# Kernel optimization log

Measured on AMD Instinct MI355X. Metric: run time of the kernel, lower is better.

The kernel has to match this reference:

```python
import jax, jax.numpy as jnp
import numpy as np

B, D, K, H = 131072, 256, 8, 128

def setup_inputs() -> dict:
    key = jax.random.key(0)
    ks = jax.random.split(key, 8)
    z = jax.random.normal(ks[0], (B, D), dtype=jnp.float32)
    logits = jax.random.normal(ks[1], (B, K), dtype=jnp.float32)
    regime_probs = jax.nn.softmax(logits, axis=-1)  # rows sum to 1, per docstring
    s1 = 1.0 / np.sqrt(D)
    s2 = 1.0 / np.sqrt(H)
    W1 = jax.random.uniform(ks[2], (K, D, H), jnp.float32, -s1, s1)
    b1 = jax.random.uniform(ks[3], (K, H), jnp.float32, -s1, s1)
    W2 = jax.random.uniform(ks[4], (K, H, H), jnp.float32, -s2, s2)
    b2 = jax.random.uniform(ks[5], (K, H), jnp.float32, -s2, s2)
    W3 = jax.random.uniform(ks[6], (K, H), jnp.float32, -s2, s2)   # final Linear(H,1) weight
    b3 = jax.random.uniform(ks[7], (K,), jnp.float32, -s2, s2)
    return {"z": z, "regime_probs": regime_probs, "W1": W1, "b1": b1,
            "W2": W2, "b2": b2, "W3": W3, "b3": b3}

def reference(z, regime_probs, W1, b1, W2, b2, W3, b3):
    # All K experts evaluated densely as grouped GEMMs (torch ran them in a Python loop).
    # GELU is exact erf-based (torch nn.GELU default). Dropout=0 -> identity.
    h = jax.nn.gelu(jnp.einsum('bd,kdh->bkh', z, W1) + b1, approximate=False)   # (B,K,H)
    h = jax.nn.gelu(jnp.einsum('bkh,khg->bkg', h, W2) + b2, approximate=False)  # (B,K,H)
    expert_preds = jnp.einsum('bkh,kh->bk', h, W3) + b3                          # (B,K)
    blended = jnp.sum(regime_probs * expert_preds, axis=1)                       # (B,)
    return (blended, expert_preds)
```

## Files before the change

kernel.cpp:

```cpp
#include <hip/hip_runtime.h>
#include <hip/hip_bf16.h>
#include <stdint.h>

#define B_ROWS 131072
#define DD 256
#define KEXP 8
#define HH 128
#define BM 64
#define NW 4

typedef float  f32x4  __attribute__((ext_vector_type(4)));
typedef short  bf16x8 __attribute__((ext_vector_type(8)));

__device__ __forceinline__ unsigned short f2bf(float f) {
    __bf16 h = (__bf16)f;
    return __builtin_bit_cast(unsigned short, h);
}

__device__ __forceinline__ float gelu_erf(float x) {
    float s = x * 0.70710678118654752f;
    float a = fabsf(s);
    float t = __builtin_amdgcn_rcpf(fmaf(0.47047f, a, 1.0f));
    float p = fmaf(t, 0.7478556f, -0.0958798f);
    p = fmaf(t, p, 0.3480242f);
    float e = __expf(-a * a);
    float Q = p * t * e;
    float sel = (s >= 0.f) ? (2.0f - Q) : Q;
    return 0.5f * x * sel;
}

__device__ __forceinline__ bf16x8 gelu_pack(f32x4 lo, f32x4 hi) {
    bf16x8 r;
    r[0] = f2bf(gelu_erf(lo[0])); r[1] = f2bf(gelu_erf(lo[1]));
    r[2] = f2bf(gelu_erf(lo[2])); r[3] = f2bf(gelu_erf(lo[3]));
    r[4] = f2bf(gelu_erf(hi[0])); r[5] = f2bf(gelu_erf(hi[1]));
    r[6] = f2bf(gelu_erf(hi[2])); r[7] = f2bf(gelu_erf(hi[3]));
    return r;
}

__global__ void convert_weights(const float* __restrict__ W1, const float* __restrict__ W2,
                                uint16_t* __restrict__ w1o, uint16_t* __restrict__ w2o) {
    int idx = blockIdx.x * blockDim.x + threadIdx.x;
    const int total1 = KEXP * HH * DD;
    if (idx < total1) {
        int k    = idx >> 15;
        int rem  = idx & 32767;
        int q    = rem >> 13;
        int r2   = rem & 8191;
        int frag = r2 >> 9;
        int r3   = r2 & 511;
        int lane = r3 >> 3;
        int j    = r3 & 7;
        int kk   = frag >> 1;
        int hb   = frag & 1;
        int g    = lane >> 4;
        int c    = lane & 15;
        int d    = kk * 32 + g * 8 + j;
        int h    = q * 32 + hb * 16 + c;
        w1o[idx] = f2bf(W1[(k * DD + d) * HH + h]);
        return;
    }
    int idx2 = idx - total1;
    const int total2 = KEXP * HH * HH;
    if (idx2 < total2) {
        int k    = idx2 >> 14;
        int rem  = idx2 & 16383;
        int half = rem >> 13;
        int r2   = rem & 8191;
        int frag = r2 >> 9;
        int r3   = r2 & 511;
        int lane = r3 >> 3;
        int j    = r3 & 7;
        int kk2  = frag >> 2;
        int blk  = frag & 3;
        int g    = lane >> 4;
        int c    = lane & 15;
        int kl   = kk2 * 32 + g * 8 + j;
        int h    = (kl & ~0x1C) | ((kl & 4) << 2) | ((kl & 0x18) >> 1);
        int g2   = half * 64 + blk * 16 + c;
        w2o[idx2] = f2bf(W2[(k * HH + h) * HH + g2]);
    }
}

__device__ __forceinline__ void stage16k(const uint16_t* __restrict__ src, uint16_t* dst,
                                         int wave, int lane) {
    const char* s = (const char*)src + wave * 1024 + lane * 16;
    char* d = (char*)dst + wave * 1024;
    #pragma unroll
    for (int i = 0; i < 4; ++i)
        __builtin_amdgcn_global_load_lds(
            (const __attribute__((address_space(1))) void*)(s + i * 4096),
            (__attribute__((address_space(3))) void*)(d + i * 4096), 16, 0, 0);
}

__global__ __launch_bounds__(256, 4)
void moe_kernel(const float* __restrict__ z, const float* __restrict__ probs,
                const float* __restrict__ b1, const float* __restrict__ b2,
                const float* __restrict__ W3, const float* __restrict__ b3,
                const uint16_t* __restrict__ w1b, const uint16_t* __restrict__ w2b,
                float* __restrict__ out) {
    __shared__ __align__(16) uint16_t wbuf[2][8192];
    __shared__ __align__(16) float preds_lds[BM * KEXP];

    const int tid  = threadIdx.x;
    const int wave = tid >> 6;
    const int lane = tid & 63;
    const int c    = lane & 15;
    const int g    = lane >> 4;
    const int wg   = blockIdx.x;
    const long rowbase = (long)wg * BM;

    bf16x8 zf[8];
    {
        const float* zr = z + (rowbase + wave * 16 + c) * DD;
        #pragma unroll
        for (int kk = 0; kk < 8; ++kk) {
            const float* p = zr + kk * 32 + g * 8;
            float4 x0 = *(const float4*)(p);
            float4 x1 = *(const float4*)(p + 4);
            bf16x8 f;
            f[0] = f2bf(x0.x); f[1] = f2bf(x0.y); f[2] = f2bf(x0.z); f[3] = f2bf(x0.w);
            f[4] = f2bf(x1.x); f[5] = f2bf(x1.y); f[6] = f2bf(x1.z); f[7] = f2bf(x1.w);
            zf[kk] = f;
        }
    }

    stage16k(w1b, wbuf[0], wave, lane);
    __syncthreads();

    int cur = 0;

    for (int ke = 0; ke < KEXP; ++ke) {
        bf16x8 pa[4];
        const uint16_t* w1e = w1b + ke * (HH * DD);
        const uint16_t* w2e = w2b + ke * (HH * HH);
        const float* bb1 = b1 + ke * HH;

        #pragma unroll
        for (int q = 0; q < 4; ++q) {
            if (q < 3) stage16k(w1e + (q + 1) * 8192, wbuf[cur ^ 1], wave, lane);
            else       stage16k(w2e,                  wbuf[cur ^ 1], wave, lane);

            f32x4 a0 = *(const f32x4*)(bb1 + 32 * q +  0 + 4 * g);
            f32x4 a1 = *(const f32x4*)(bb1 + 32 * q + 16 + 4 * g);
            const bf16x8* fb = (const bf16x8*)(wbuf[cur]) + lane;
            #pragma unroll
            for (int kk = 0; kk < 8; ++kk) {
                a0 = __builtin_amdgcn_mfma_f32_16x16x32_bf16(fb[kk * 128     ], zf[kk], a0, 0, 0, 0);
                a1 = __builtin_amdgcn_mfma_f32_16x16x32_bf16(fb[kk * 128 + 64], zf[kk], a1, 0, 0, 0);
            }
            pa[q] = gelu_pack(a0, a1);
            __syncthreads(); cur ^= 1;
        }

        f32x4 q0, q1, q2, q3;
        {
            stage16k(w2e + 8192, wbuf[cur ^ 1], wave, lane);
            const float* bb2 = b2 + ke * HH;
            q0 = *(const f32x4*)(bb2 +  0 + 4 * g);
            q1 = *(const f32x4*)(bb2 + 16 + 4 * g);
            q2 = *(const f32x4*)(bb2 + 32 + 4 * g);
            q3 = *(const f32x4*)(bb2 + 48 + 4 * g);
            const bf16x8* fb = (const bf16x8*)(wbuf[cur]) + lane;
            #pragma unroll
            for (int kk2 = 0; kk2 < 4; ++kk2) {
                q0 = __builtin_amdgcn_mfma_f32_16x16x32_bf16(fb[kk2 * 256      ], pa[kk2], q0, 0, 0, 0);
                q1 = __builtin_amdgcn_mfma_f32_16x16x32_bf16(fb[kk2 * 256 +  64], pa[kk2], q1, 0, 0, 0);
                q2 = __builtin_amdgcn_mfma_f32_16x16x32_bf16(fb[kk2 * 256 + 128], pa[kk2], q2, 0, 0, 0);
                q3 = __builtin_amdgcn_mfma_f32_16x16x32_bf16(fb[kk2 * 256 + 192], pa[kk2], q3, 0, 0, 0);
            }
            __syncthreads(); cur ^= 1;
        }

        {
            if (ke + 1 < KEXP) stage16k(w1b + (ke + 1) * (HH * DD), wbuf[cur ^ 1], wave, lane);
            const float* bb2 = b2 + ke * HH + 64;
            f32x4 q4 = *(const f32x4*)(bb2 +  0 + 4 * g);
            f32x4 q5 = *(const f32x4*)(bb2 + 16 + 4 * g);
            f32x4 q6 = *(const f32x4*)(bb2 + 32 + 4 * g);
            f32x4 q7 = *(const f32x4*)(bb2 + 48 + 4 * g);
            const bf16x8* fb = (const bf16x8*)(wbuf[cur]) + lane;
            #pragma unroll
            for (int kk2 = 0; kk2 < 4; ++kk2) {
                q4 = __builtin_amdgcn_mfma_f32_16x16x32_bf16(fb[kk2 * 256      ], pa[kk2], q4, 0, 0, 0);
                q5 = __builtin_amdgcn_mfma_f32_16x16x32_bf16(fb[kk2 * 256 +  64], pa[kk2], q5, 0, 0, 0);
                q6 = __builtin_amdgcn_mfma_f32_16x16x32_bf16(fb[kk2 * 256 + 128], pa[kk2], q6, 0, 0, 0);
                q7 = __builtin_amdgcn_mfma_f32_16x16x32_bf16(fb[kk2 * 256 + 192], pa[kk2], q7, 0, 0, 0);
            }

            const float* w3p = W3 + ke * HH;
            float part = 0.f;
            f32x4 w3v;
            #define DOT(qq, off) \
                w3v = *(const f32x4*)(w3p + off + 4 * g); \
                part = fmaf(gelu_erf(qq[0]), w3v[0], part); \
                part = fmaf(gelu_erf(qq[1]), w3v[1], part); \
                part = fmaf(gelu_erf(qq[2]), w3v[2], part); \
                part = fmaf(gelu_erf(qq[3]), w3v[3], part);
            DOT(q0,   0) DOT(q1,  16) DOT(q2,  32) DOT(q3,  48)
            DOT(q4,  64) DOT(q5,  80) DOT(q6,  96) DOT(q7, 112)
            #undef DOT
            part += __shfl_xor(part, 16);
            part += __shfl_xor(part, 32);
            if (g == 0)
                preds_lds[(wave * 16 + c) * KEXP + ke] = part + b3[ke];
            __syncthreads(); cur ^= 1;
        }
    }

    {
        float2 v = *(const float2*)(preds_lds + tid * 2);
        *(float2*)(out + B_ROWS + rowbase * KEXP + tid * 2) = v;
    }
    if (tid < BM) {
        const float* pr = probs + (rowbase + tid) * KEXP;
        float4 p0 = *(const float4*)(pr);
        float4 p1 = *(const float4*)(pr + 4);
        const float* pd = preds_lds + tid * KEXP;
        float s = 0.f;
        s = fmaf(p0.x, pd[0], s); s = fmaf(p0.y, pd[1], s);
        s = fmaf(p0.z, pd[2], s); s = fmaf(p0.w, pd[3], s);
        s = fmaf(p1.x, pd[4], s); s = fmaf(p1.y, pd[5], s);
        s = fmaf(p1.z, pd[6], s); s = fmaf(p1.w, pd[7], s);
        out[rowbase + tid] = s;
    }
}

extern "C" void kernel_launch(void* const* d_in, const int* in_sizes, int n_in,
                              void* d_out, int out_size, void* d_ws, size_t ws_size,
                              hipStream_t stream) {
    const float* z     = (const float*)d_in[0];
    const float* probs = (const float*)d_in[1];
    const float* W1    = (const float*)d_in[2];
    const float* b1    = (const float*)d_in[3];
    const float* W2    = (const float*)d_in[4];
    const float* b2    = (const float*)d_in[5];
    const float* W3    = (const float*)d_in[6];
    const float* b3    = (const float*)d_in[7];
    float* out = (float*)d_out;

    uint16_t* w1b = (uint16_t*)d_ws;
    uint16_t* w2b = w1b + (size_t)KEXP * HH * DD;

    const int totalw = KEXP * HH * DD + KEXP * HH * HH;
    convert_weights<<<(totalw + 255) / 256, 256, 0, stream>>>(W1, W2, w1b, w2b);
    moe_kernel<<<B_ROWS / BM, 256, 0, stream>>>(z, probs, b1, b2, W3, b3, w1b, w2b, out);
}
```

Measured before the change: 208.0 us.

## Double rows per workgroup so each LDS weight fragment feeds two MFMA tiles

Each wave now handles 32 rows as two 16-row tiles, A and B. Every weight fragment read from LDS feeds two MFMAs, which halves the weight staging and LDS traffic per row and halves the workgroup count. The first-half layer-3 dot product moves into the first W2 phase, so those accumulators are consumed earlier and register pressure drops. In exchange each thread holds more registers, and launch bounds fall from 4 to 3 waves per SIMD, which reduces occupancy.

```diff
diff --git a/kernel.cpp b/kernel.cpp
--- a/kernel.cpp
+++ b/kernel.cpp
@@ -6,7 +6,7 @@
 #define DD 256
 #define KEXP 8
 #define HH 128
-#define BM 64
+#define BM 128
 #define NW 4
 
 typedef float  f32x4  __attribute__((ext_vector_type(4)));
@@ -93,7 +93,7 @@
             (__attribute__((address_space(3))) void*)(d + i * 4096), 16, 0, 0);
 }
 
-__global__ __launch_bounds__(256, 4)
+__global__ __launch_bounds__(256, 3)
 void moe_kernel(const float* __restrict__ z, const float* __restrict__ probs,
                 const float* __restrict__ b1, const float* __restrict__ b2,
                 const float* __restrict__ W3, const float* __restrict__ b3,
@@ -110,18 +110,25 @@
     const int wg   = blockIdx.x;
     const long rowbase = (long)wg * BM;
 
-    bf16x8 zf[8];
+    bf16x8 zfA[8], zfB[8];
     {
-        const float* zr = z + (rowbase + wave * 16 + c) * DD;
+        const float* zrA = z + (rowbase + wave * 32 + c) * DD;
+        const float* zrB = zrA + 16 * DD;
         #pragma unroll
         for (int kk = 0; kk < 8; ++kk) {
-            const float* p = zr + kk * 32 + g * 8;
-            float4 x0 = *(const float4*)(p);
-            float4 x1 = *(const float4*)(p + 4);
+            const float* pA = zrA + kk * 32 + g * 8;
+            const float* pB = zrB + kk * 32 + g * 8;
+            float4 x0 = *(const float4*)(pA);
+            float4 x1 = *(const float4*)(pA + 4);
             bf16x8 f;
             f[0] = f2bf(x0.x); f[1] = f2bf(x0.y); f[2] = f2bf(x0.z); f[3] = f2bf(x0.w);
             f[4] = f2bf(x1.x); f[5] = f2bf(x1.y); f[6] = f2bf(x1.z); f[7] = f2bf(x1.w);
-            zf[kk] = f;
+            zfA[kk] = f;
+            x0 = *(const float4*)(pB);
+            x1 = *(const float4*)(pB + 4);
+            f[0] = f2bf(x0.x); f[1] = f2bf(x0.y); f[2] = f2bf(x0.z); f[3] = f2bf(x0.w);
+            f[4] = f2bf(x1.x); f[5] = f2bf(x1.y); f[6] = f2bf(x1.z); f[7] = f2bf(x1.w);
+            zfB[kk] = f;
         }
     }
 
@@ -131,7 +138,7 @@
     int cur = 0;
 
     for (int ke = 0; ke < KEXP; ++ke) {
-        bf16x8 pa[4];
+        bf16x8 paA[4], paB[4];
         const uint16_t* w1e = w1b + ke * (HH * DD);
         const uint16_t* w2e = w2b + ke * (HH * HH);
         const float* bb1 = b1 + ke * HH;
@@ -141,76 +148,112 @@
             if (q < 3) stage16k(w1e + (q + 1) * 8192, wbuf[cur ^ 1], wave, lane);
             else       stage16k(w2e,                  wbuf[cur ^ 1], wave, lane);
 
-            f32x4 a0 = *(const f32x4*)(bb1 + 32 * q +  0 + 4 * g);
-            f32x4 a1 = *(const f32x4*)(bb1 + 32 * q + 16 + 4 * g);
+            f32x4 b0 = *(const f32x4*)(bb1 + 32 * q +  0 + 4 * g);
+            f32x4 b1v = *(const f32x4*)(bb1 + 32 * q + 16 + 4 * g);
+            f32x4 a0A = b0, a1A = b1v, a0B = b0, a1B = b1v;
             const bf16x8* fb = (const bf16x8*)(wbuf[cur]) + lane;
             #pragma unroll
             for (int kk = 0; kk < 8; ++kk) {
-                a0 = __builtin_amdgcn_mfma_f32_16x16x32_bf16(fb[kk * 128     ], zf[kk], a0, 0, 0, 0);
-                a1 = __builtin_amdgcn_mfma_f32_16x16x32_bf16(fb[kk * 128 + 64], zf[kk], a1, 0, 0, 0);
-            }
-            pa[q] = gelu_pack(a0, a1);
+                bf16x8 f0 = fb[kk * 128];
+                bf16x8 f1 = fb[kk * 128 + 64];
+                a0A = __builtin_amdgcn_mfma_f32_16x16x32_bf16(f0, zfA[kk], a0A, 0, 0, 0);
+                a0B = __builtin_amdgcn_mfma_f32_16x16x32_bf16(f0, zfB[kk], a0B, 0, 0, 0);
+                a1A = __builtin_amdgcn_mfma_f32_16x16x32_bf16(f1, zfA[kk], a1A, 0, 0, 0);
+                a1B = __builtin_amdgcn_mfma_f32_16x16x32_bf16(f1, zfB[kk], a1B, 0, 0, 0);
+            }
+            paA[q] = gelu_pack(a0A, a1A);
+            paB[q] = gelu_pack(a0B, a1B);
             __syncthreads(); cur ^= 1;
         }
 
-        f32x4 q0, q1, q2, q3;
+        float partA = 0.f, partB = 0.f;
+
         {
             stage16k(w2e + 8192, wbuf[cur ^ 1], wave, lane);
             const float* bb2 = b2 + ke * HH;
-            q0 = *(const f32x4*)(bb2 +  0 + 4 * g);
-            q1 = *(const f32x4*)(bb2 + 16 + 4 * g);
-            q2 = *(const f32x4*)(bb2 + 32 + 4 * g);
-            q3 = *(const f32x4*)(bb2 + 48 + 4 * g);
+            f32x4 c0 = *(const f32x4*)(bb2 +  0 + 4 * g);
+            f32x4 c1 = *(const f32x4*)(bb2 + 16 + 4 * g);
+            f32x4 c2 = *(const f32x4*)(bb2 + 32 + 4 * g);
+            f32x4 c3 = *(const f32x4*)(bb2 + 48 + 4 * g);
+            f32x4 q0A = c0, q1A = c1, q2A = c2, q3A = c3;
+            f32x4 q0B = c0, q1B = c1, q2B = c2, q3B = c3;
             const bf16x8* fb = (const bf16x8*)(wbuf[cur]) + lane;
             #pragma unroll
             for (int kk2 = 0; kk2 < 4; ++kk2) {
-                q0 = __builtin_amdgcn_mfma_f32_16x16x32_bf16(fb[kk2 * 256      ], pa[kk2], q0, 0, 0, 0);
-                q1 = __builtin_amdgcn_mfma_f32_16x16x32_bf16(fb[kk2 * 256 +  64], pa[kk2], q1, 0, 0, 0);
-                q2 = __builtin_amdgcn_mfma_f32_16x16x32_bf16(fb[kk2 * 256 + 128], pa[kk2], q2, 0, 0, 0);
-                q3 = __builtin_amdgcn_mfma_f32_16x16x32_bf16(fb[kk2 * 256 + 192], pa[kk2], q3, 0, 0, 0);
-            }
+                bf16x8 f0 = fb[kk2 * 256      ];
+                bf16x8 f1 = fb[kk2 * 256 +  64];
+                bf16x8 f2 = fb[kk2 * 256 + 128];
+                bf16x8 f3 = fb[kk2 * 256 + 192];
+                q0A = __builtin_amdgcn_mfma_f32_16x16x32_bf16(f0, paA[kk2], q0A, 0, 0, 0);
+                q0B = __builtin_amdgcn_mfma_f32_16x16x32_bf16(f0, paB[kk2], q0B, 0, 0, 0);
+                q1A = __builtin_amdgcn_mfma_f32_16x16x32_bf16(f1, paA[kk2], q1A, 0, 0, 0);
+                q1B = __builtin_amdgcn_mfma_f32_16x16x32_bf16(f1, paB[kk2], q1B, 0, 0, 0);
+                q2A = __builtin_amdgcn_mfma_f32_16x16x32_bf16(f2, paA[kk2], q2A, 0, 0, 0);
+                q2B = __builtin_amdgcn_mfma_f32_16x16x32_bf16(f2, paB[kk2], q2B, 0, 0, 0);
+                q3A = __builtin_amdgcn_mfma_f32_16x16x32_bf16(f3, paA[kk2], q3A, 0, 0, 0);
+                q3B = __builtin_amdgcn_mfma_f32_16x16x32_bf16(f3, paB[kk2], q3B, 0, 0, 0);
+            }
+            const float* w3p = W3 + ke * HH;
+            f32x4 w3v;
+            #define DOT2(qa, qb, off) \
+                w3v = *(const f32x4*)(w3p + off + 4 * g); \
+                partA = fmaf(gelu_erf(qa[0]), w3v[0], partA); \
+                partA = fmaf(gelu_erf(qa[1]), w3v[1], partA); \
+                partA = fmaf(gelu_erf(qa[2]), w3v[2], partA); \
+                partA = fmaf(gelu_erf(qa[3]), w3v[3], partA); \
+                partB = fmaf(gelu_erf(qb[0]), w3v[0], partB); \
+                partB = fmaf(gelu_erf(qb[1]), w3v[1], partB); \
+                partB = fmaf(gelu_erf(qb[2]), w3v[2], partB); \
+                partB = fmaf(gelu_erf(qb[3]), w3v[3], partB);
+            DOT2(q0A, q0B,  0) DOT2(q1A, q1B, 16) DOT2(q2A, q2B, 32) DOT2(q3A, q3B, 48)
             __syncthreads(); cur ^= 1;
         }
 
         {
             if (ke + 1 < KEXP) stage16k(w1b + (ke + 1) * (HH * DD), wbuf[cur ^ 1], wave, lane);
             const float* bb2 = b2 + ke * HH + 64;
-            f32x4 q4 = *(const f32x4*)(bb2 +  0 + 4 * g);
-            f32x4 q5 = *(const f32x4*)(bb2 + 16 + 4 * g);
-            f32x4 q6 = *(const f32x4*)(bb2 + 32 + 4 * g);
-            f32x4 q7 = *(const f32x4*)(bb2 + 48 + 4 * g);
+            f32x4 c0 = *(const f32x4*)(bb2 +  0 + 4 * g);
+            f32x4 c1 = *(const f32x4*)(bb2 + 16 + 4 * g);
+            f32x4 c2 = *(const f32x4*)(bb2 + 32 + 4 * g);
+            f32x4 c3 = *(const f32x4*)(bb2 + 48 + 4 * g);
+            f32x4 q4A = c0, q5A = c1, q6A = c2, q7A = c3;
+            f32x4 q4B = c0, q5B = c1, q6B = c2, q7B = c3;
             const bf16x8* fb = (const bf16x8*)(wbuf[cur]) + lane;
             #pragma unroll
             for (int kk2 = 0; kk2 < 4; ++kk2) {
-                q4 = __builtin_amdgcn_mfma_f32_16x16x32_bf16(fb[kk2 * 256      ], pa[kk2], q4, 0, 0, 0);
-                q5 = __builtin_amdgcn_mfma_f32_16x16x32_bf16(fb[kk2 * 256 +  64], pa[kk2], q5, 0, 0, 0);
-                q6 = __builtin_amdgcn_mfma_f32_16x16x32_bf16(fb[kk2 * 256 + 128], pa[kk2], q6, 0, 0, 0);
-                q7 = __builtin_amdgcn_mfma_f32_16x16x32_bf16(fb[kk2 * 256 + 192], pa[kk2], q7, 0, 0, 0);
-            }
-
-            const float* w3p = W3 + ke * HH;
-            float part = 0.f;
+                bf16x8 f0 = fb[kk2 * 256      ];
+                bf16x8 f1 = fb[kk2 * 256 +  64];
+                bf16x8 f2 = fb[kk2 * 256 + 128];
+                bf16x8 f3 = fb[kk2 * 256 + 192];
+                q4A = __builtin_amdgcn_mfma_f32_16x16x32_bf16(f0, paA[kk2], q4A, 0, 0, 0);
+                q4B = __builtin_amdgcn_mfma_f32_16x16x32_bf16(f0, paB[kk2], q4B, 0, 0, 0);
+                q5A = __builtin_amdgcn_mfma_f32_16x16x32_bf16(f1, paA[kk2], q5A, 0, 0, 0);
+                q5B = __builtin_amdgcn_mfma_f32_16x16x32_bf16(f1, paB[kk2], q5B, 0, 0, 0);
+                q6A = __builtin_amdgcn_mfma_f32_16x16x32_bf16(f2, paA[kk2], q6A, 0, 0, 0);
+                q6B = __builtin_amdgcn_mfma_f32_16x16x32_bf16(f2, paB[kk2], q6B, 0, 0, 0);
+                q7A = __builtin_amdgcn_mfma_f32_16x16x32_bf16(f3, paA[kk2], q7A, 0, 0, 0);
+                q7B = __builtin_amdgcn_mfma_f32_16x16x32_bf16(f3, paB[kk2], q7B, 0, 0, 0);
+            }
+            const float* w3p = W3 + ke * HH + 64;
             f32x4 w3v;
-            #define DOT(qq, off) \
-                w3v = *(const f32x4*)(w3p + off + 4 * g); \
-                part = fmaf(gelu_erf(qq[0]), w3v[0], part); \
-                part = fmaf(gelu_erf(qq[1]), w3v[1], part); \
-                part = fmaf(gelu_erf(qq[2]), w3v[2], part); \
-                part = fmaf(gelu_erf(qq[3]), w3v[3], part);
-            DOT(q0,   0) DOT(q1,  16) DOT(q2,  32) DOT(q3,  48)
-            DOT(q4,  64) DOT(q5,  80) DOT(q6,  96) DOT(q7, 112)
-            #undef DOT
-            part += __shfl_xor(part, 16);
-            part += __shfl_xor(part, 32);
-            if (g == 0)
-                preds_lds[(wave * 16 + c) * KEXP + ke] = part + b3[ke];
+            DOT2(q4A, q4B,  0) DOT2(q5A, q5B, 16) DOT2(q6A, q6B, 32) DOT2(q7A, q7B, 48)
+            #undef DOT2
+            partA += __shfl_xor(partA, 16);
+            partA += __shfl_xor(partA, 32);
+            partB += __shfl_xor(partB, 16);
+            partB += __shfl_xor(partB, 32);
+            if (g == 0) {
+                float b3v = b3[ke];
+                preds_lds[(wave * 32 + c) * KEXP + ke]      = partA + b3v;
+                preds_lds[(wave * 32 + 16 + c) * KEXP + ke] = partB + b3v;
+            }
             __syncthreads(); cur ^= 1;
         }
     }
 
     {
-        float2 v = *(const float2*)(preds_lds + tid * 2);
-        *(float2*)(out + B_ROWS + rowbase * KEXP + tid * 2) = v;
+        float4 v = *(const float4*)(preds_lds + tid * 4);
+        *(float4*)(out + B_ROWS + rowbase * KEXP + tid * 4) = v;
     }
     if (tid < BM) {
         const float* pr = probs + (rowbase + tid) * KEXP;
```

After: 328.2 us. 1.58x slower.
